# Performance work log

Measured on AMD Instinct MI355X. Metric: run time of the kernel, lower is better.

## Reference

```python
import jax, jax.numpy as jnp
import numpy as np

TEMP = 0.1
EPS = 1e-12  # torch F.normalize eps


def _normalize(v):
    return v / jnp.maximum(jnp.linalg.norm(v, axis=1, keepdims=True), EPS)


def _scale_loss(a1, a2, b1, c1):
    # diag of exp(a1 @ a2.T / temp): computed directly from paired rows
    # (same math as eye-mask + row-sum in the original).
    diag = jnp.exp(jnp.sum(a1 * a2, axis=1) / TEMP)            # [B]
    denom = (jnp.exp(a1 @ b1.T / TEMP).sum(1, keepdims=True)
             + jnp.exp(a1 @ c1.T / TEMP).sum(1, keepdims=True))  # [B,1]
    # NOTE: [B] / [B,1] broadcasts to [B,B], exactly as in the torch code.
    return jnp.mean(-jnp.log(diag / denom))


def setup_inputs() -> dict:
    key = jax.random.key(0)
    kx, ky, kz = jax.random.split(key, 3)
    shape = (8192, 128)
    return {
        "x": jax.random.normal(kx, shape, dtype=jnp.float32),
        "y": jax.random.normal(ky, shape, dtype=jnp.float32),
        "z": jax.random.normal(kz, shape, dtype=jnp.float32),
    }


def reference(x, y, z):
    x = _normalize(x)
    y = _normalize(y)
    z = _normalize(z)
    B = x.shape[0] // 2
    x1, x2 = x[:B], x[B:]
    y1, y2 = y[:B], y[B:]
    z1, z2 = z[:B], z[B:]

    loss_scale = (_scale_loss(x1, x2, y1, z1)
                  + _scale_loss(y1, y2, x1, z1)
                  + _scale_loss(z1, z2, x1, y1))

    xyz1 = jnp.concatenate([x1, y1, z1], axis=1)  # [B, 3D]
    xyz2 = jnp.concatenate([x2, y2, z2], axis=1)
    m = jnp.exp(xyz1 @ xyz2.T / TEMP)             # [B, B]
    # [B] / [B,1] -> [B,B] broadcast, matching the torch code.
    loss_view = jnp.mean(-jnp.log(jnp.diagonal(m) / m.sum(1, keepdims=True)))

    return loss_view + loss_scale
```

## Files before the change

kernel.cpp:

```cpp
#include <hip/hip_runtime.h>
#include <hip/hip_bf16.h>

#define BHALF 4096
#define DDIM 128
#define KCAT 384
#define TEMP_INV 10.0f

typedef __attribute__((ext_vector_type(8))) short short8;
typedef __attribute__((ext_vector_type(4))) float f32x4;

__device__ __forceinline__ void gload16(const ushort* g, ushort* l) {
  __builtin_amdgcn_global_load_lds(
      (const __attribute__((address_space(1))) unsigned int*)g,
      (__attribute__((address_space(3))) unsigned int*)l, 16, 0, 0);
}

__global__ __launch_bounds__(256) void norm_diag_kernel(
    const float* __restrict__ x, const float* __restrict__ y,
    const float* __restrict__ z, ushort* __restrict__ nrm1,
    ushort* __restrict__ nrm2, float* __restrict__ dxyz) {
  int wave = threadIdx.x >> 6;
  int lane = threadIdx.x & 63;
  int gi = blockIdx.x * 4 + wave;
  int mat = gi >> 12;
  int i = gi & 4095;
  const float* src = (mat == 0 ? x : (mat == 1 ? y : z));
  float2 a = *(const float2*)(src + (size_t)i * DDIM + lane * 2);
  float2 b = *(const float2*)(src + (size_t)(i + BHALF) * DDIM + lane * 2);
  float s1 = a.x * a.x + a.y * a.y;
  float s2 = b.x * b.x + b.y * b.y;
  float d = a.x * b.x + a.y * b.y;
#pragma unroll
  for (int m = 1; m < 64; m <<= 1) {
    s1 += __shfl_xor(s1, m, 64);
    s2 += __shfl_xor(s2, m, 64);
    d += __shfl_xor(d, m, 64);
  }
  float r1 = 1.0f / fmaxf(sqrtf(s1), 1e-12f);
  float r2 = 1.0f / fmaxf(sqrtf(s2), 1e-12f);
  ushort* d1 = nrm1 + (size_t)i * KCAT + mat * DDIM + lane * 2;
  ushort* d2 = nrm2 + (size_t)i * KCAT + mat * DDIM + lane * 2;
  __hip_bfloat162 o1, o2;
  o1.x = __float2bfloat16(a.x * r1);
  o1.y = __float2bfloat16(a.y * r1);
  o2.x = __float2bfloat16(b.x * r2);
  o2.y = __float2bfloat16(b.y * r2);
  *(__hip_bfloat162*)d1 = o1;
  *(__hip_bfloat162*)d2 = o2;
  if (lane == 0) dxyz[mat * BHALF + i] = d * r1 * r2;
}

__global__ __launch_bounds__(256) void gram_kernel(
    const ushort* __restrict__ nrm1, const ushort* __restrict__ nrm2,
    float* __restrict__ sums) {
  int g = blockIdx.z;
  const ushort* Abase;
  const ushort* Bbase;
  int K;
  float* rs;
  float* cs;
  if (g == 0) {
    Abase = nrm1; Bbase = nrm1 + 128; K = 128;
    rs = sums; cs = sums + 4096;
  } else if (g == 1) {
    Abase = nrm1; Bbase = nrm1 + 256; K = 128;
    rs = sums + 2 * 4096; cs = sums + 3 * 4096;
  } else if (g == 2) {
    Abase = nrm1 + 128; Bbase = nrm1 + 256; K = 128;
    rs = sums + 4 * 4096; cs = sums + 5 * 4096;
  } else {
    Abase = nrm1; Bbase = nrm2; K = 384;
    rs = sums + 6 * 4096; cs = nullptr;
  }

  __shared__ ushort As[2][128][32];
  __shared__ ushort Bs[2][128][32];

  int tid = threadIdx.x;
  int lane = tid & 63;
  int wave = tid >> 6;
  int wr = wave >> 1;
  int wc = wave & 1;

  int rowbase = blockIdx.x * 128;
  int colbase = blockIdx.y * 128;

  int lrow = lane >> 2;
  int lchunk8 = (((lane & 3) ^ ((lrow >> 1) & 3)) << 3);
  const ushort* gA =
      Abase + (size_t)(rowbase + wave * 16 + lrow) * KCAT + lchunk8;
  const ushort* gB =
      Bbase + (size_t)(colbase + wave * 16 + lrow) * KCAT + lchunk8;

  int rsel = lane & 15;
  int slot8 = (((lane >> 4) ^ ((rsel >> 1) & 3)) << 3);

  f32x4 acc[4][4] = {};

  int ksteps = K >> 5;

#define STAGE(b, t)                                        \
  do {                                                     \
    const ushort* a_ = gA + (t) * 32;                      \
    const ushort* b_ = gB + (t) * 32;                      \
    gload16(a_, &As[(b)][wave * 16][0]);                   \
    gload16(a_ + (size_t)64 * KCAT, &As[(b)][wave * 16 + 64][0]); \
    gload16(b_, &Bs[(b)][wave * 16][0]);                   \
    gload16(b_ + (size_t)64 * KCAT, &Bs[(b)][wave * 16 + 64][0]); \
  } while (0)

  STAGE(0, 0);
  for (int t = 0; t < ksteps; ++t) {
    int cur = t & 1;
    if (t + 1 < ksteps) {
      STAGE(cur ^ 1, t + 1);
      asm volatile("s_waitcnt vmcnt(4)" ::: "memory");
    } else {
      asm volatile("s_waitcnt vmcnt(0)" ::: "memory");
    }
    __builtin_amdgcn_s_barrier();
    __builtin_amdgcn_sched_barrier(0);
    short8 af[4], bf[4];
#pragma unroll
    for (int m = 0; m < 4; ++m)
      af[m] = *(const short8*)&As[cur][wr * 64 + m * 16 + rsel][slot8];
#pragma unroll
    for (int n = 0; n < 4; ++n)
      bf[n] = *(const short8*)&Bs[cur][wc * 64 + n * 16 + rsel][slot8];
#pragma unroll
    for (int m = 0; m < 4; ++m)
#pragma unroll
      for (int n = 0; n < 4; ++n)
        acc[m][n] = __builtin_amdgcn_mfma_f32_16x16x32_bf16(af[m], bf[n],
                                                            acc[m][n], 0, 0, 0);
    __builtin_amdgcn_sched_barrier(0);
    __builtin_amdgcn_s_barrier();
  }
#undef STAGE

#pragma unroll
  for (int m = 0; m < 4; ++m)
#pragma unroll
    for (int n = 0; n < 4; ++n)
#pragma unroll
      for (int r = 0; r < 4; ++r)
        acc[m][n][r] = __expf(acc[m][n][r] * TEMP_INV);

#pragma unroll
  for (int m = 0; m < 4; ++m) {
    float rsum[4];
#pragma unroll
    for (int r = 0; r < 4; ++r)
      rsum[r] = acc[m][0][r] + acc[m][1][r] + acc[m][2][r] + acc[m][3][r];
#pragma unroll
    for (int r = 0; r < 4; ++r) {
      rsum[r] += __shfl_xor(rsum[r], 1, 64);
      rsum[r] += __shfl_xor(rsum[r], 2, 64);
      rsum[r] += __shfl_xor(rsum[r], 4, 64);
      rsum[r] += __shfl_xor(rsum[r], 8, 64);
    }
    if ((lane & 15) == 0) {
      int rbase = rowbase + wr * 64 + m * 16 + (lane >> 4) * 4;
#pragma unroll
      for (int r = 0; r < 4; ++r) atomicAdd(&rs[rbase + r], rsum[r]);
    }
  }

  if (cs != nullptr) {
#pragma unroll
    for (int n = 0; n < 4; ++n) {
      float csum = 0.0f;
#pragma unroll
      for (int m = 0; m < 4; ++m)
#pragma unroll
        for (int r = 0; r < 4; ++r) csum += acc[m][n][r];
      csum += __shfl_xor(csum, 16, 64);
      csum += __shfl_xor(csum, 32, 64);
      if (lane < 16) atomicAdd(&cs[colbase + wc * 64 + n * 16 + lane], csum);
    }
  }
}

__global__ __launch_bounds__(1024) void loss_kernel(
    const float* __restrict__ sums, const float* __restrict__ dxyz,
    float* __restrict__ out) {
  const float* rs0 = sums;
  const float* cs0 = sums + 4096;
  const float* rs1 = sums + 2 * 4096;
  const float* cs1 = sums + 3 * 4096;
  const float* rs2 = sums + 4 * 4096;
  const float* cs2 = sums + 5 * 4096;
  const float* rs3 = sums + 6 * 4096;
  int tid = threadIdx.x;
  float acc = 0.0f;
  for (int i = tid; i < BHALF; i += 1024) {
    float dxv = dxyz[i];
    float dyv = dxyz[4096 + i];
    float dzv = dxyz[2 * 4096 + i];
    float lx = logf(rs0[i] + rs1[i]) - TEMP_INV * dxv;
    float ly = logf(cs0[i] + rs2[i]) - TEMP_INV * dyv;
    float lz = logf(cs1[i] + cs2[i]) - TEMP_INV * dzv;
    float lv = logf(rs3[i]) - TEMP_INV * (dxv + dyv + dzv);
    acc += lx + ly + lz + lv;
  }
  __shared__ float red[16];
#pragma unroll
  for (int m = 1; m < 64; m <<= 1) acc += __shfl_xor(acc, m, 64);
  if ((tid & 63) == 0) red[tid >> 6] = acc;
  __syncthreads();
  if (tid == 0) {
    float t = 0.0f;
#pragma unroll
    for (int i = 0; i < 16; ++i) t += red[i];
    out[0] = t * (1.0f / 4096.0f);
  }
}

extern "C" void kernel_launch(void* const* d_in, const int* in_sizes, int n_in,
                              void* d_out, int out_size, void* d_ws,
                              size_t ws_size, hipStream_t stream) {
  const float* x = (const float*)d_in[0];
  const float* y = (const float*)d_in[1];
  const float* z = (const float*)d_in[2];
  char* ws = (char*)d_ws;
  ushort* nrm1 = (ushort*)ws;
  ushort* nrm2 = nrm1 + (size_t)BHALF * KCAT;
  float* sums = (float*)(ws + 2 * (size_t)BHALF * KCAT * sizeof(ushort));
  float* dxyz = sums + 7 * 4096;

  hipMemsetAsync(sums, 0, 7 * 4096 * sizeof(float), stream);
  norm_diag_kernel<<<3 * BHALF / 4, 256, 0, stream>>>(x, y, z, nrm1, nrm2,
                                                      dxyz);
  gram_kernel<<<dim3(32, 32, 4), 256, 0, stream>>>(nrm1, nrm2, sums);
  loss_kernel<<<1, 1024, 0, stream>>>(sums, dxyz, (float*)d_out);
}
```

Baseline: 81.71 us.

## Fuse four gram GEMMs into one persistent tile loop with per-segment flushes

Replaces the 4-slice grid (one z-slice per gram product) with a single 32x32 grid where each block walks all four K-segments (384 for the view GEMM, then three 128-wide cross GEMMs) in one fully unrolled 24-step pipeline. After each segment it applies exp, does the row/column reductions and atomics, then zeroes the accumulators. The aim is to keep the load pipeline running across segments, cut block launch/prologue overhead, and reuse cached A rows. In exchange there are 4x fewer blocks (1024 over the CUs), so parallelism drops and the flush epilogues sit serially inside the loop, and the full unroll increases code size and register pressure.

Result: slower. 109.0 us (+33.4%).

```diff
diff --git a/kernel.cpp b/kernel.cpp
--- a/kernel.cpp
+++ b/kernel.cpp
@@ -50,29 +50,62 @@
   if (lane == 0) dxyz[mat * BHALF + i] = d * r1 * r2;
 }
 
-__global__ __launch_bounds__(256) void gram_kernel(
+__device__ __forceinline__ void flush_gram(f32x4 (&acc)[4][4], float* rs,
+                                           float* cs, int rowbase, int colbase,
+                                           int wr, int wc, int lane) {
+#pragma unroll
+  for (int m = 0; m < 4; ++m)
+#pragma unroll
+    for (int n = 0; n < 4; ++n)
+#pragma unroll
+      for (int r = 0; r < 4; ++r)
+        acc[m][n][r] = __expf(acc[m][n][r] * TEMP_INV);
+
+#pragma unroll
+  for (int m = 0; m < 4; ++m) {
+    float rsum[4];
+#pragma unroll
+    for (int r = 0; r < 4; ++r)
+      rsum[r] = acc[m][0][r] + acc[m][1][r] + acc[m][2][r] + acc[m][3][r];
+#pragma unroll
+    for (int r = 0; r < 4; ++r) {
+      rsum[r] += __shfl_xor(rsum[r], 1, 64);
+      rsum[r] += __shfl_xor(rsum[r], 2, 64);
+      rsum[r] += __shfl_xor(rsum[r], 4, 64);
+      rsum[r] += __shfl_xor(rsum[r], 8, 64);
+    }
+    if ((lane & 15) == 0) {
+      int rbase = rowbase + wr * 64 + m * 16 + (lane >> 4) * 4;
+#pragma unroll
+      for (int r = 0; r < 4; ++r) atomicAdd(&rs[rbase + r], rsum[r]);
+    }
+  }
+
+  if (cs != nullptr) {
+#pragma unroll
+    for (int n = 0; n < 4; ++n) {
+      float csum = 0.0f;
+#pragma unroll
+      for (int m = 0; m < 4; ++m)
+#pragma unroll
+        for (int r = 0; r < 4; ++r) csum += acc[m][n][r];
+      csum += __shfl_xor(csum, 16, 64);
+      csum += __shfl_xor(csum, 32, 64);
+      if (lane < 16) atomicAdd(&cs[colbase + wc * 64 + n * 16 + lane], csum);
+    }
+  }
+
+#pragma unroll
+  for (int m = 0; m < 4; ++m)
+#pragma unroll
+    for (int n = 0; n < 4; ++n)
+#pragma unroll
+      for (int r = 0; r < 4; ++r) acc[m][n][r] = 0.0f;
+}
+
+__global__ __launch_bounds__(256) void gram_fused_kernel(
     const ushort* __restrict__ nrm1, const ushort* __restrict__ nrm2,
     float* __restrict__ sums) {
-  int g = blockIdx.z;
-  const ushort* Abase;
-  const ushort* Bbase;
-  int K;
-  float* rs;
-  float* cs;
-  if (g == 0) {
-    Abase = nrm1; Bbase = nrm1 + 128; K = 128;
-    rs = sums; cs = sums + 4096;
-  } else if (g == 1) {
-    Abase = nrm1; Bbase = nrm1 + 256; K = 128;
-    rs = sums + 2 * 4096; cs = sums + 3 * 4096;
-  } else if (g == 2) {
-    Abase = nrm1 + 128; Bbase = nrm1 + 256; K = 128;
-    rs = sums + 4 * 4096; cs = sums + 5 * 4096;
-  } else {
-    Abase = nrm1; Bbase = nrm2; K = 384;
-    rs = sums + 6 * 4096; cs = nullptr;
-  }
-
   __shared__ ushort As[2][128][32];
   __shared__ ushort Bs[2][128][32];
 
@@ -88,31 +121,41 @@
   int lrow = lane >> 2;
   int lchunk8 = (((lane & 3) ^ ((lrow >> 1) & 3)) << 3);
   const ushort* gA =
-      Abase + (size_t)(rowbase + wave * 16 + lrow) * KCAT + lchunk8;
-  const ushort* gB =
-      Bbase + (size_t)(colbase + wave * 16 + lrow) * KCAT + lchunk8;
+      nrm1 + (size_t)(rowbase + wave * 16 + lrow) * KCAT + lchunk8;
+  const ushort* gB1 =
+      nrm1 + (size_t)(colbase + wave * 16 + lrow) * KCAT + lchunk8;
+  const ushort* gB2 =
+      nrm2 + (size_t)(colbase + wave * 16 + lrow) * KCAT + lchunk8;
 
   int rsel = lane & 15;
   int slot8 = (((lane >> 4) ^ ((rsel >> 1) & 3)) << 3);
 
   f32x4 acc[4][4] = {};
 
-  int ksteps = K >> 5;
-
-#define STAGE(b, t)                                        \
-  do {                                                     \
-    const ushort* a_ = gA + (t) * 32;                      \
-    const ushort* b_ = gB + (t) * 32;                      \
-    gload16(a_, &As[(b)][wave * 16][0]);                   \
-    gload16(a_ + (size_t)64 * KCAT, &As[(b)][wave * 16 + 64][0]); \
-    gload16(b_, &Bs[(b)][wave * 16][0]);                   \
-    gload16(b_ + (size_t)64 * KCAT, &Bs[(b)][wave * 16 + 64][0]); \
+#define AOFF(t)                                                      \
+  ((t) < 12 ? (t) * 32                                               \
+            : (t) < 16 ? ((t)-12) * 32                               \
+                       : (t) < 20 ? ((t)-16) * 32 : ((t)-20) * 32 + 128)
+#define BPTR(t)                                                      \
+  ((t) < 12 ? gB2 + (t) * 32                                         \
+            : (t) < 16 ? gB1 + 128 + ((t)-12) * 32                   \
+                       : (t) < 20 ? gB1 + 256 + ((t)-16) * 32        \
+                                  : gB1 + 256 + ((t)-20) * 32)
+#define STAGE(b, t)                                                  \
+  do {                                                               \
+    const ushort* a_ = gA + AOFF(t);                                 \
+    const ushort* b_ = BPTR(t);                                      \
+    gload16(a_, &As[(b)][wave * 16][0]);                             \
+    gload16(a_ + (size_t)64 * KCAT, &As[(b)][wave * 16 + 64][0]);    \
+    gload16(b_, &Bs[(b)][wave * 16][0]);                             \
+    gload16(b_ + (size_t)64 * KCAT, &Bs[(b)][wave * 16 + 64][0]);    \
   } while (0)
 
   STAGE(0, 0);
-  for (int t = 0; t < ksteps; ++t) {
+#pragma unroll
+  for (int t = 0; t < 24; ++t) {
     int cur = t & 1;
-    if (t + 1 < ksteps) {
+    if (t < 23) {
       STAGE(cur ^ 1, t + 1);
       asm volatile("s_waitcnt vmcnt(4)" ::: "memory");
     } else {
@@ -133,52 +176,22 @@
       for (int n = 0; n < 4; ++n)
         acc[m][n] = __builtin_amdgcn_mfma_f32_16x16x32_bf16(af[m], bf[n],
                                                             acc[m][n], 0, 0, 0);
-    __builtin_amdgcn_sched_barrier(0);
     __builtin_amdgcn_s_barrier();
+
+    if (t == 11)
+      flush_gram(acc, sums + 6 * 4096, nullptr, rowbase, colbase, wr, wc, lane);
+    else if (t == 15)
+      flush_gram(acc, sums, sums + 4096, rowbase, colbase, wr, wc, lane);
+    else if (t == 19)
+      flush_gram(acc, sums + 2 * 4096, sums + 3 * 4096, rowbase, colbase, wr,
+                 wc, lane);
+    else if (t == 23)
+      flush_gram(acc, sums + 4 * 4096, sums + 5 * 4096, rowbase, colbase, wr,
+                 wc, lane);
   }
 #undef STAGE
-
-#pragma unroll
-  for (int m = 0; m < 4; ++m)
-#pragma unroll
-    for (int n = 0; n < 4; ++n)
-#pragma unroll
-      for (int r = 0; r < 4; ++r)
-        acc[m][n][r] = __expf(acc[m][n][r] * TEMP_INV);
-
-#pragma unroll
-  for (int m = 0; m < 4; ++m) {
-    float rsum[4];
-#pragma unroll
-    for (int r = 0; r < 4; ++r)
-      rsum[r] = acc[m][0][r] + acc[m][1][r] + acc[m][2][r] + acc[m][3][r];
-#pragma unroll
-    for (int r = 0; r < 4; ++r) {
-      rsum[r] += __shfl_xor(rsum[r], 1, 64);
-      rsum[r] += __shfl_xor(rsum[r], 2, 64);
-      rsum[r] += __shfl_xor(rsum[r], 4, 64);
-      rsum[r] += __shfl_xor(rsum[r], 8, 64);
-    }
-    if ((lane & 15) == 0) {
-      int rbase = rowbase + wr * 64 + m * 16 + (lane >> 4) * 4;
-#pragma unroll
-      for (int r = 0; r < 4; ++r) atomicAdd(&rs[rbase + r], rsum[r]);
-    }
-  }
-
-  if (cs != nullptr) {
-#pragma unroll
-    for (int n = 0; n < 4; ++n) {
-      float csum = 0.0f;
-#pragma unroll
-      for (int m = 0; m < 4; ++m)
-#pragma unroll
-        for (int r = 0; r < 4; ++r) csum += acc[m][n][r];
-      csum += __shfl_xor(csum, 16, 64);
-      csum += __shfl_xor(csum, 32, 64);
-      if (lane < 16) atomicAdd(&cs[colbase + wc * 64 + n * 16 + lane], csum);
-    }
-  }
+#undef BPTR
+#undef AOFF
 }
 
 __global__ __launch_bounds__(1024) void loss_kernel(
@@ -231,6 +244,6 @@
   hipMemsetAsync(sums, 0, 7 * 4096 * sizeof(float), stream);
   norm_diag_kernel<<<3 * BHALF / 4, 256, 0, stream>>>(x, y, z, nrm1, nrm2,
                                                       dxyz);
-  gram_kernel<<<dim3(32, 32, 4), 256, 0, stream>>>(nrm1, nrm2, sums);
+  gram_fused_kernel<<<dim3(32, 32), 256, 0, stream>>>(nrm1, nrm2, sums);
   loss_kernel<<<1, 1024, 0, stream>>>(sums, dxyz, (float*)d_out);
 }
```
